# Performance work log

Hardware: AMD Instinct MI355X
Metric: run time of the kernel (lower is better)

The kernel has to match this reference:

```python
import jax, jax.numpy as jnp
import numpy as np

TGT, BSZ, E = 256, 8, 256
SRC = 4096
H = 8
HD = E // H


def setup_inputs() -> dict:
    key = jax.random.key(0)
    ks = jax.random.split(key, 6)
    return {
        "query": jax.random.normal(ks[0], (TGT, BSZ, E), dtype=jnp.float32),
        "key": jax.random.normal(ks[1], (SRC, BSZ, E), dtype=jnp.float32),
        "value": jax.random.normal(ks[2], (SRC, BSZ, E), dtype=jnp.float32),
        "proposal_mask": jax.random.uniform(ks[3], (BSZ, TGT, SRC), dtype=jnp.float32),
        "out_proj_weight": jax.random.normal(ks[4], (E, E), dtype=jnp.float32) * (1.0 / np.sqrt(E)),
        "out_proj_bias": jax.random.normal(ks[5], (E,), dtype=jnp.float32) * 0.01,
    }


def reference(query, key, value, proposal_mask, out_proj_weight, out_proj_bias):
    tgt_len, bsz, embed_dim = query.shape
    src_len = key.shape[0]
    num_heads = H
    head_dim = embed_dim // num_heads

    # v: (src, bsz, E) -> (src, bsz*H, hd) -> (bsz*H, src, hd); index q = b*H + h
    v = value.reshape(src_len, bsz * num_heads, head_dim).transpose(1, 0, 2)

    # proposal_mask (bsz, tgt, src); torch loop+stack produces mask_nhead[b*H+h] = proposal_mask[b]
    mask_nhead = jnp.repeat(proposal_mask, num_heads, axis=0)  # (bsz*H, tgt, src)

    # weighted sum of values per head (no score compute)
    attn_output = jnp.einsum('qts,qsc->qtc', mask_nhead, v)  # (bsz*H, tgt, hd)

    # (bsz*H, tgt, hd) -> (tgt, bsz*H, hd) -> (tgt, bsz, E)
    attn_output = attn_output.transpose(1, 0, 2).reshape(tgt_len, bsz, embed_dim)

    # out projection (outDecoderLayer=False)
    attn_output = attn_output @ out_proj_weight.T + out_proj_bias

    # averaged weights: mask repeated per head -> mean over heads == proposal_mask
    attn_weights = mask_nhead.reshape(bsz, num_heads, tgt_len, src_len).sum(axis=1) / num_heads
    return attn_output, attn_weights
```

## Files before the change

### kernel.cpp

```cpp
#include <hip/hip_runtime.h>
#include <hip/hip_bf16.h>

#define TGT 256
#define BSZ 8
#define E   256
#define SRC 4096

typedef __attribute__((ext_vector_type(8))) short           bf16x8;
typedef __attribute__((ext_vector_type(4))) float           f32x4;
typedef __attribute__((ext_vector_type(4))) float           f4;
typedef __attribute__((ext_vector_type(4))) unsigned short  u16x4;

__device__ inline unsigned short f2b(float x) {
    union { __hip_bfloat16 h; unsigned short u; } cv;
    cv.h = __float2bfloat16(x);
    return cv.u;
}

__device__ inline bf16x8 cvt8v(const float* __restrict__ p) {
    f4 lo = *(const f4*)p;
    f4 hi = *(const f4*)(p + 4);
    bf16x8 r;
    #pragma unroll
    for (int j = 0; j < 4; ++j) {
        r[j]     = (short)f2b(lo[j]);
        r[4 + j] = (short)f2b(hi[j]);
    }
    return r;
}

#define AP 136
#define VP 40

__global__ __launch_bounds__(512) void gemm1_fused(
    const float* __restrict__ value,
    const float* __restrict__ mask,
    float* __restrict__ out1,
    float* __restrict__ part)
{
    __shared__ unsigned short As[2][32 * AP];
    __shared__ unsigned short Vs[2][256 * VP];

    const int bx  = blockIdx.x;
    const int b   = bx & 7;
    const int tt  = (bx >> 3) & 7;
    const int kc  = bx >> 6;
    const int t0  = tt * 32;
    const int k0  = kc * 1024;
    const int tid = threadIdx.x;
    const int w    = tid >> 6;
    const int lane = tid & 63;
    const int quad = lane >> 4;
    const int l15  = lane & 15;

    const int sr0 = tid >> 5;
    const int sr1 = sr0 + 16;
    const int sc  = (tid & 31) * 4;
    const float* mbase = mask + (size_t)b * TGT * SRC + (size_t)t0 * SRC + k0;
    float*       obase = out1 + (size_t)b * TGT * SRC + (size_t)t0 * SRC + k0;

    const int ve  = tid & 255;
    const int vkg = (tid >> 8) * 16;
    const float* vbase = value + (size_t)k0 * (BSZ * E) + (size_t)b * E + ve;

    f32x4 acc00 = {}, acc01 = {}, acc10 = {}, acc11 = {};

    {
        f4 v0 = *(const f4*)(mbase + (size_t)sr0 * SRC + sc);
        f4 v1 = *(const f4*)(mbase + (size_t)sr1 * SRC + sc);
        *(f4*)(obase + (size_t)sr0 * SRC + sc) = v0;
        *(f4*)(obase + (size_t)sr1 * SRC + sc) = v1;
        unsigned short* d0 = &As[0][sr0 * AP + sc];
        unsigned short* d1 = &As[0][sr1 * AP + sc];
        #pragma unroll
        for (int j = 0; j < 4; ++j) { d0[j] = f2b(v0[j]); d1[j] = f2b(v1[j]); }

        const float* vp = vbase + (size_t)vkg * (BSZ * E);
        float vv[16];
        #pragma unroll
        for (int i = 0; i < 16; ++i) vv[i] = vp[(size_t)i * (BSZ * E)];
        #pragma unroll
        for (int g = 0; g < 4; ++g) {
            u16x4 pk;
            #pragma unroll
            for (int c = 0; c < 4; ++c) pk[c] = f2b(vv[g * 4 + c]);
            *(u16x4*)&Vs[0][ve * VP + vkg + g * 4] = pk;
        }
    }
    __syncthreads();

    for (int s = 0; s < 32; ++s) {
        const int vb = s & 1;
        const int ab = (s >> 2) & 1;
        const int haveV = (s < 31);
        const int haveA = ((s & 3) == 0) && (s < 28);

        float vv[16];
        if (haveV) {
            const float* vp = vbase + (size_t)((s + 1) * 32 + vkg) * (BSZ * E);
            #pragma unroll
            for (int i = 0; i < 16; ++i) vv[i] = vp[(size_t)i * (BSZ * E)];
        }
        f4 a0v, a1v;
        if (haveA) {
            int ka = ((s >> 2) + 1) * 128;
            a0v = *(const f4*)(mbase + (size_t)sr0 * SRC + ka + sc);
            a1v = *(const f4*)(mbase + (size_t)sr1 * SRC + ka + sc);
        }

        {
            const int koff = (s & 3) * 32 + quad * 8;
            bf16x8 a0 = *(const bf16x8*)&As[ab][ l15       * AP + koff];
            bf16x8 a1 = *(const bf16x8*)&As[ab][(l15 + 16) * AP + koff];
            bf16x8 b0 = *(const bf16x8*)&Vs[vb][(w * 32 + l15)      * VP + quad * 8];
            bf16x8 b1 = *(const bf16x8*)&Vs[vb][(w * 32 + l15 + 16) * VP + quad * 8];
            acc00 = __builtin_amdgcn_mfma_f32_16x16x32_bf16(a0, b0, acc00, 0, 0, 0);
            acc01 = __builtin_amdgcn_mfma_f32_16x16x32_bf16(a0, b1, acc01, 0, 0, 0);
            acc10 = __builtin_amdgcn_mfma_f32_16x16x32_bf16(a1, b0, acc10, 0, 0, 0);
            acc11 = __builtin_amdgcn_mfma_f32_16x16x32_bf16(a1, b1, acc11, 0, 0, 0);
        }

        if (haveA) {
            int ka = ((s >> 2) + 1) * 128;
            *(f4*)(obase + (size_t)sr0 * SRC + ka + sc) = a0v;
            *(f4*)(obase + (size_t)sr1 * SRC + ka + sc) = a1v;
            unsigned short* d0 = &As[ab ^ 1][sr0 * AP + sc];
            unsigned short* d1 = &As[ab ^ 1][sr1 * AP + sc];
            #pragma unroll
            for (int j = 0; j < 4; ++j) { d0[j] = f2b(a0v[j]); d1[j] = f2b(a1v[j]); }
        }
        if (haveV) {
            #pragma unroll
            for (int g = 0; g < 4; ++g) {
                u16x4 pk;
                #pragma unroll
                for (int c = 0; c < 4; ++c) pk[c] = f2b(vv[g * 4 + c]);
                *(u16x4*)&Vs[vb ^ 1][ve * VP + vkg + g * 4] = pk;
            }
        }
        __syncthreads();
    }

    float* pb = part + ((size_t)kc * BSZ + b) * TGT * E;
    #pragma unroll
    for (int r = 0; r < 4; ++r) {
        int rr0 = t0 + quad * 4 + r;
        int rr1 = rr0 + 16;
        int c0  = w * 32 + l15;
        pb[(size_t)rr0 * E + c0]      = acc00[r];
        pb[(size_t)rr0 * E + c0 + 16] = acc01[r];
        pb[(size_t)rr1 * E + c0]      = acc10[r];
        pb[(size_t)rr1 * E + c0 + 16] = acc11[r];
    }
}

#define PSTRIDE ((size_t)BSZ * TGT * E)

__global__ __launch_bounds__(256) void gemm2(
    const float* __restrict__ part,
    const float* __restrict__ wgt,
    const float* __restrict__ bias,
    float* __restrict__ out0)
{
    const int tid  = threadIdx.x;
    const int wv   = tid >> 6;
    const int lane = tid & 63;
    const int tau  = blockIdx.x * 4 + wv;
    const int b    = tau >> 8;
    const int rem  = tau & 255;
    const int t0   = (rem >> 4) * 16;
    const int e0   = (rem & 15) * 16;
    const int quad = lane >> 4;
    const int l15  = lane & 15;

    const float* arow = part + (size_t)b * TGT * E + (size_t)(t0 + l15) * E + quad * 8;
    const float* brow = wgt + (size_t)(e0 + l15) * E + quad * 8;

    f32x4 acc = {};
    #pragma unroll
    for (int ks = 0; ks < 8; ++ks) {
        const float* ap = arow + ks * 32;
        f4 lo = *(const f4*)(ap);
        f4 hi = *(const f4*)(ap + 4);
        #pragma unroll
        for (int p = 1; p < 4; ++p) {
            lo += *(const f4*)(ap + p * PSTRIDE);
            hi += *(const f4*)(ap + p * PSTRIDE + 4);
        }
        bf16x8 a;
        #pragma unroll
        for (int j = 0; j < 4; ++j) {
            a[j]     = (short)f2b(lo[j]);
            a[4 + j] = (short)f2b(hi[j]);
        }
        bf16x8 bb = cvt8v(brow + ks * 32);
        acc = __builtin_amdgcn_mfma_f32_16x16x32_bf16(a, bb, acc, 0, 0, 0);
    }

    const float bval = bias[e0 + l15];
    #pragma unroll
    for (int r = 0; r < 4; ++r) {
        int t = t0 + quad * 4 + r;
        int e = e0 + l15;
        out0[(size_t)t * (BSZ * E) + (size_t)b * E + e] = acc[r] + bval;
    }
}

extern "C" void kernel_launch(void* const* d_in, const int* in_sizes, int n_in,
                              void* d_out, int out_size, void* d_ws, size_t ws_size,
                              hipStream_t stream)
{
    const float* value = (const float*)d_in[2];
    const float* mask  = (const float*)d_in[3];
    const float* wgt   = (const float*)d_in[4];
    const float* bias  = (const float*)d_in[5];

    float* out0 = (float*)d_out;
    float* out1 = (float*)d_out + (size_t)TGT * BSZ * E;

    float* part = (float*)d_ws;

    gemm1_fused<<<256, 512, 0, stream>>>(value, mask, out1, part);
    gemm2<<<512, 256, 0, stream>>>(part, wgt, bias, out0);
}
```

Measured before the change: 178.3 us.

## Prepack V and W into bf16 MFMA fragments, split K finer, separate reduction

Adds pre-pass kernels that convert value and the out-projection weight into bf16 MFMA-fragment layout in workspace, so gemm1 loads B fragments directly from global memory instead of doing strided fp32 loads, conversion and LDS staging. gemm1 now splits K into 8 chunks of 512 (512 blocks) to raise parallelism, and a new reduce kernel sums the 8 partials and emits bf16 A fragments for gemm2. The cost is three extra launches and extra workspace traffic for the fragment buffers and the doubled partial-sum storage.

```diff
diff --git a/kernel.cpp b/kernel.cpp
--- a/kernel.cpp
+++ b/kernel.cpp
@@ -9,7 +9,7 @@
 typedef __attribute__((ext_vector_type(8))) short           bf16x8;
 typedef __attribute__((ext_vector_type(4))) float           f32x4;
 typedef __attribute__((ext_vector_type(4))) float           f4;
-typedef __attribute__((ext_vector_type(4))) unsigned short  u16x4;
+typedef __attribute__((ext_vector_type(8))) unsigned short  u16x8;
 
 __device__ inline unsigned short f2b(float x) {
     union { __hip_bfloat16 h; unsigned short u; } cv;
@@ -22,48 +22,86 @@
     f4 hi = *(const f4*)(p + 4);
     bf16x8 r;
     #pragma unroll
-    for (int j = 0; j < 4; ++j) {
-        r[j]     = (short)f2b(lo[j]);
-        r[4 + j] = (short)f2b(hi[j]);
-    }
+    for (int j = 0; j < 4; ++j) { r[j] = (short)f2b(lo[j]); r[4 + j] = (short)f2b(hi[j]); }
     return r;
 }
 
+__global__ __launch_bounds__(256) void v_frag(
+    const float* __restrict__ value, unsigned short* __restrict__ vtf)
+{
+    __shared__ unsigned short tile[64 * 264];
+    const int kch = blockIdx.x;
+    const int b   = blockIdx.y;
+    const int k0  = kch * 64;
+    const int tid = threadIdx.x;
+
+    #pragma unroll
+    for (int i = 0; i < 16; ++i) {
+        int lin = i * 256 + tid;
+        int row = lin >> 6;
+        int c4  = lin & 63;
+        f4 v = *(const f4*)(value + (size_t)(k0 + row) * (BSZ * E)
+                                  + (size_t)b * E + c4 * 4);
+        #pragma unroll
+        for (int j = 0; j < 4; ++j) tile[row * 264 + c4 * 4 + j] = f2b(v[j]);
+    }
+    __syncthreads();
+
+    #pragma unroll
+    for (int i = 0; i < 8; ++i) {
+        int o    = i * 256 + tid;
+        int et   = o >> 7;
+        int ksl  = (o >> 6) & 1;
+        int lane = o & 63;
+        int quad = lane >> 4, l15 = lane & 15;
+        u16x8 pk;
+        #pragma unroll
+        for (int j = 0; j < 8; ++j)
+            pk[j] = tile[(ksl * 32 + quad * 8 + j) * 264 + et * 16 + l15];
+        size_t ks = (size_t)kch * 2 + ksl;
+        *(u16x8*)&vtf[((((size_t)b * 16 + et) * 128 + ks) * 64 + lane) * 8] = pk;
+    }
+}
+
+__global__ __launch_bounds__(256) void w_frag(
+    const float* __restrict__ wgt, unsigned short* __restrict__ wf)
+{
+    int o    = blockIdx.x * 256 + threadIdx.x;
+    int et   = o >> 9;
+    int ks   = (o >> 6) & 7;
+    int lane = o & 63;
+    int quad = lane >> 4, l15 = lane & 15;
+    bf16x8 v = cvt8v(wgt + (size_t)(et * 16 + l15) * E + ks * 32 + quad * 8);
+    *(bf16x8*)&wf[(size_t)o * 8] = v;
+}
+
 #define AP 136
-#define VP 40
-
-__global__ __launch_bounds__(512) void gemm1_fused(
-    const float* __restrict__ value,
+
+__global__ __launch_bounds__(512) void gemm1(
     const float* __restrict__ mask,
+    const unsigned short* __restrict__ vtf,
     float* __restrict__ out1,
     float* __restrict__ part)
 {
     __shared__ unsigned short As[2][32 * AP];
-    __shared__ unsigned short Vs[2][256 * VP];
-
     const int bx  = blockIdx.x;
     const int b   = bx & 7;
     const int tt  = (bx >> 3) & 7;
     const int kc  = bx >> 6;
     const int t0  = tt * 32;
-    const int k0  = kc * 1024;
+    const int k0  = kc * 512;
     const int tid = threadIdx.x;
     const int w    = tid >> 6;
     const int lane = tid & 63;
     const int quad = lane >> 4;
     const int l15  = lane & 15;
 
-    const int sr0 = tid >> 5;
-    const int sr1 = sr0 + 16;
-    const int sc  = (tid & 31) * 4;
     const float* mbase = mask + (size_t)b * TGT * SRC + (size_t)t0 * SRC + k0;
     float*       obase = out1 + (size_t)b * TGT * SRC + (size_t)t0 * SRC + k0;
-
-    const int ve  = tid & 255;
-    const int vkg = (tid >> 8) * 16;
-    const float* vbase = value + (size_t)k0 * (BSZ * E) + (size_t)b * E + ve;
-
-    f32x4 acc00 = {}, acc01 = {}, acc10 = {}, acc11 = {};
+    const int sr0 = tid >> 5, sr1 = sr0 + 16, sc = (tid & 31) * 4;
+
+    const unsigned short* bfr0 = vtf + (((size_t)b * 16 + 2 * w) * 128 + (size_t)kc * 16) * 512;
+    const unsigned short* bfr1 = bfr0 + (size_t)128 * 512;
 
     {
         f4 v0 = *(const f4*)(mbase + (size_t)sr0 * SRC + sc);
@@ -74,69 +112,36 @@
         unsigned short* d1 = &As[0][sr1 * AP + sc];
         #pragma unroll
         for (int j = 0; j < 4; ++j) { d0[j] = f2b(v0[j]); d1[j] = f2b(v1[j]); }
-
-        const float* vp = vbase + (size_t)vkg * (BSZ * E);
-        float vv[16];
-        #pragma unroll
-        for (int i = 0; i < 16; ++i) vv[i] = vp[(size_t)i * (BSZ * E)];
-        #pragma unroll
-        for (int g = 0; g < 4; ++g) {
-            u16x4 pk;
-            #pragma unroll
-            for (int c = 0; c < 4; ++c) pk[c] = f2b(vv[g * 4 + c]);
-            *(u16x4*)&Vs[0][ve * VP + vkg + g * 4] = pk;
+    }
+    __syncthreads();
+
+    f32x4 acc00 = {}, acc01 = {}, acc10 = {}, acc11 = {};
+
+    #pragma unroll
+    for (int s = 0; s < 4; ++s) {
+        f4 a0v, a1v;
+        if (s < 3) {
+            a0v = *(const f4*)(mbase + (size_t)sr0 * SRC + (s + 1) * 128 + sc);
+            a1v = *(const f4*)(mbase + (size_t)sr1 * SRC + (s + 1) * 128 + sc);
         }
-    }
-    __syncthreads();
-
-    for (int s = 0; s < 32; ++s) {
-        const int vb = s & 1;
-        const int ab = (s >> 2) & 1;
-        const int haveV = (s < 31);
-        const int haveA = ((s & 3) == 0) && (s < 28);
-
-        float vv[16];
-        if (haveV) {
-            const float* vp = vbase + (size_t)((s + 1) * 32 + vkg) * (BSZ * E);
-            #pragma unroll
-            for (int i = 0; i < 16; ++i) vv[i] = vp[(size_t)i * (BSZ * E)];
+        #pragma unroll
+        for (int q = 0; q < 4; ++q) {
+            bf16x8 B0 = *(const bf16x8*)(bfr0 + ((size_t)(s * 4 + q) * 64 + lane) * 8);
+            bf16x8 B1 = *(const bf16x8*)(bfr1 + ((size_t)(s * 4 + q) * 64 + lane) * 8);
+            bf16x8 a0 = *(const bf16x8*)&As[s & 1][ l15       * AP + q * 32 + quad * 8];
+            bf16x8 a1 = *(const bf16x8*)&As[s & 1][(l15 + 16) * AP + q * 32 + quad * 8];
+            acc00 = __builtin_amdgcn_mfma_f32_16x16x32_bf16(a0, B0, acc00, 0, 0, 0);
+            acc01 = __builtin_amdgcn_mfma_f32_16x16x32_bf16(a0, B1, acc01, 0, 0, 0);
+            acc10 = __builtin_amdgcn_mfma_f32_16x16x32_bf16(a1, B0, acc10, 0, 0, 0);
+            acc11 = __builtin_amdgcn_mfma_f32_16x16x32_bf16(a1, B1, acc11, 0, 0, 0);
         }
-        f4 a0v, a1v;
-        if (haveA) {
-            int ka = ((s >> 2) + 1) * 128;
-            a0v = *(const f4*)(mbase + (size_t)sr0 * SRC + ka + sc);
-            a1v = *(const f4*)(mbase + (size_t)sr1 * SRC + ka + sc);
-        }
-
-        {
-            const int koff = (s & 3) * 32 + quad * 8;
-            bf16x8 a0 = *(const bf16x8*)&As[ab][ l15       * AP + koff];
-            bf16x8 a1 = *(const bf16x8*)&As[ab][(l15 + 16) * AP + koff];
-            bf16x8 b0 = *(const bf16x8*)&Vs[vb][(w * 32 + l15)      * VP + quad * 8];
-            bf16x8 b1 = *(const bf16x8*)&Vs[vb][(w * 32 + l15 + 16) * VP + quad * 8];
-            acc00 = __builtin_amdgcn_mfma_f32_16x16x32_bf16(a0, b0, acc00, 0, 0, 0);
-            acc01 = __builtin_amdgcn_mfma_f32_16x16x32_bf16(a0, b1, acc01, 0, 0, 0);
-            acc10 = __builtin_amdgcn_mfma_f32_16x16x32_bf16(a1, b0, acc10, 0, 0, 0);
-            acc11 = __builtin_amdgcn_mfma_f32_16x16x32_bf16(a1, b1, acc11, 0, 0, 0);
-        }
-
-        if (haveA) {
-            int ka = ((s >> 2) + 1) * 128;
-            *(f4*)(obase + (size_t)sr0 * SRC + ka + sc) = a0v;
-            *(f4*)(obase + (size_t)sr1 * SRC + ka + sc) = a1v;
-            unsigned short* d0 = &As[ab ^ 1][sr0 * AP + sc];
-            unsigned short* d1 = &As[ab ^ 1][sr1 * AP + sc];
+        if (s < 3) {
+            *(f4*)(obase + (size_t)sr0 * SRC + (s + 1) * 128 + sc) = a0v;
+            *(f4*)(obase + (size_t)sr1 * SRC + (s + 1) * 128 + sc) = a1v;
+            unsigned short* d0 = &As[(s + 1) & 1][sr0 * AP + sc];
+            unsigned short* d1 = &As[(s + 1) & 1][sr1 * AP + sc];
             #pragma unroll
             for (int j = 0; j < 4; ++j) { d0[j] = f2b(a0v[j]); d1[j] = f2b(a1v[j]); }
-        }
-        if (haveV) {
-            #pragma unroll
-            for (int g = 0; g < 4; ++g) {
-                u16x4 pk;
-                #pragma unroll
-                for (int c = 0; c < 4; ++c) pk[c] = f2b(vv[g * 4 + c]);
-                *(u16x4*)&Vs[vb ^ 1][ve * VP + vkg + g * 4] = pk;
-            }
         }
         __syncthreads();
     }
@@ -156,9 +161,33 @@
 
 #define PSTRIDE ((size_t)BSZ * TGT * E)
 
+__global__ __launch_bounds__(256) void reduce_part(
+    const float* __restrict__ part, unsigned short* __restrict__ credf)
+{
+    int o    = blockIdx.x * 256 + threadIdx.x;
+    int b    = o >> 13;
+    int tt16 = (o >> 9) & 15;
+    int ks   = (o >> 6) & 7;
+    int lane = o & 63;
+    int quad = lane >> 4, l15 = lane & 15;
+    const float* ap = part + (size_t)b * TGT * E
+                    + (size_t)(tt16 * 16 + l15) * E + ks * 32 + quad * 8;
+    f4 lo = *(const f4*)ap;
+    f4 hi = *(const f4*)(ap + 4);
+    #pragma unroll
+    for (int p = 1; p < 8; ++p) {
+        lo += *(const f4*)(ap + p * PSTRIDE);
+        hi += *(const f4*)(ap + p * PSTRIDE + 4);
+    }
+    u16x8 pk;
+    #pragma unroll
+    for (int j = 0; j < 4; ++j) { pk[j] = f2b(lo[j]); pk[4 + j] = f2b(hi[j]); }
+    *(u16x8*)&credf[(size_t)o * 8] = pk;
+}
+
 __global__ __launch_bounds__(256) void gemm2(
-    const float* __restrict__ part,
-    const float* __restrict__ wgt,
+    const unsigned short* __restrict__ credf,
+    const unsigned short* __restrict__ wf,
     const float* __restrict__ bias,
     float* __restrict__ out0)
 {
@@ -168,40 +197,27 @@
     const int tau  = blockIdx.x * 4 + wv;
     const int b    = tau >> 8;
     const int rem  = tau & 255;
-    const int t0   = (rem >> 4) * 16;
-    const int e0   = (rem & 15) * 16;
+    const int tt16 = rem >> 4;
+    const int et   = rem & 15;
     const int quad = lane >> 4;
     const int l15  = lane & 15;
 
-    const float* arow = part + (size_t)b * TGT * E + (size_t)(t0 + l15) * E + quad * 8;
-    const float* brow = wgt + (size_t)(e0 + l15) * E + quad * 8;
+    const unsigned short* af = credf + (((size_t)b * 16 + tt16) * 8) * 512 + (size_t)lane * 8;
+    const unsigned short* bf = wf + ((size_t)et * 8) * 512 + (size_t)lane * 8;
 
     f32x4 acc = {};
     #pragma unroll
     for (int ks = 0; ks < 8; ++ks) {
-        const float* ap = arow + ks * 32;
-        f4 lo = *(const f4*)(ap);
-        f4 hi = *(const f4*)(ap + 4);
-        #pragma unroll
-        for (int p = 1; p < 4; ++p) {
-            lo += *(const f4*)(ap + p * PSTRIDE);
-            hi += *(const f4*)(ap + p * PSTRIDE + 4);
-        }
-        bf16x8 a;
-        #pragma unroll
-        for (int j = 0; j < 4; ++j) {
-            a[j]     = (short)f2b(lo[j]);
-            a[4 + j] = (short)f2b(hi[j]);
-        }
-        bf16x8 bb = cvt8v(brow + ks * 32);
+        bf16x8 a  = *(const bf16x8*)(af + (size_t)ks * 512);
+        bf16x8 bb = *(const bf16x8*)(bf + (size_t)ks * 512);
         acc = __builtin_amdgcn_mfma_f32_16x16x32_bf16(a, bb, acc, 0, 0, 0);
     }
 
-    const float bval = bias[e0 + l15];
+    const float bval = bias[et * 16 + l15];
     #pragma unroll
     for (int r = 0; r < 4; ++r) {
-        int t = t0 + quad * 4 + r;
-        int e = e0 + l15;
+        int t = tt16 * 16 + quad * 4 + r;
+        int e = et * 16 + l15;
         out0[(size_t)t * (BSZ * E) + (size_t)b * E + e] = acc[r] + bval;
     }
 }
@@ -218,8 +234,14 @@
     float* out0 = (float*)d_out;
     float* out1 = (float*)d_out + (size_t)TGT * BSZ * E;
 
-    float* part = (float*)d_ws;
-
-    gemm1_fused<<<256, 512, 0, stream>>>(value, mask, out1, part);
-    gemm2<<<512, 256, 0, stream>>>(part, wgt, bias, out0);
-}
+    unsigned short* vtf   = (unsigned short*)d_ws;
+    unsigned short* wf    = vtf + (size_t)BSZ * E * SRC;
+    float*          part  = (float*)(wf + (size_t)16 * 8 * 64 * 8);
+    unsigned short* credf = (unsigned short*)(part + (size_t)8 * BSZ * TGT * E);
+
+    v_frag<<<dim3(64, BSZ), 256, 0, stream>>>(value, vtf);
+    w_frag<<<32, 256, 0, stream>>>(wgt, wf);
+    gemm1<<<512, 512, 0, stream>>>(mask, vtf, out1, part);
+    reduce_part<<<256, 256, 0, stream>>>(part, credf);
+    gemm2<<<512, 256, 0, stream>>>(credf, wf, bias, out0);
+}
```

Result: faster. 152.8 us (-14.3%).
